# Performance work log

Measured on AMD Instinct MI355X. Metric: run time of the kernel, lower is better.

## Reference

```python
import jax, jax.numpy as jnp
import numpy as np

B, S, E, H, L = 16, 1024, 512, 8, 4
D = E // H  # head_dim = 64


def setup_inputs() -> dict:
    key = jax.random.key(0)
    ks = jax.random.split(key, 16)
    std = 0.02
    inp = {
        "q": jax.random.normal(ks[0], (B, S, E), jnp.float32),
        "k": jax.random.normal(ks[1], (B, S, E), jnp.float32),
        "v": jax.random.normal(ks[2], (B, S, E), jnp.float32),
        # standard Linear params (torch convention: W is (out, in))
        "Wq": jax.random.normal(ks[3], (E, E), jnp.float32) * std,
        "bq": jnp.zeros((E,), jnp.float32),
        "Wk": jax.random.normal(ks[4], (E, E), jnp.float32) * std,
        "bk": jnp.zeros((E,), jnp.float32),
        # WFLinear: shared weight elementwise-multiplied by per-language factor
        "Wv_share": jax.random.normal(ks[5], (E, E), jnp.float32) * std,
        "Wv_spec": 1.0 + jax.random.normal(ks[6], (L, E, E), jnp.float32) * std,
        "bv_share": jnp.zeros((E,), jnp.float32),
        "bv_spec": jax.random.normal(ks[7], (L, E), jnp.float32) * std,
        "Wo_share": jax.random.normal(ks[8], (E, E), jnp.float32) * std,
        "Wo_spec": 1.0 + jax.random.normal(ks[9], (L, E, E), jnp.float32) * std,
        "bo_share": jnp.zeros((E,), jnp.float32),
        "bo_spec": jax.random.normal(ks[10], (L, E), jnp.float32) * std,
        "mask": jax.random.randint(ks[11], (B, S), 0, 2, jnp.int32),
        "languageID": 1,
    }
    return inp


def reference(q, k, v, Wq, bq, Wk, bk, Wv_share, Wv_spec, bv_share, bv_spec,
              Wo_share, Wo_spec, bo_share, bo_spec, mask, languageID):
    scaling = D ** (-0.5)
    # projections (torch Linear: x @ W.T + b)
    Q = (q @ Wq.T + bq).reshape(B, S, H, D).transpose(0, 2, 1, 3) * scaling
    K = (k @ Wk.T + bk).reshape(B, S, H, D).transpose(0, 2, 1, 3)
    Wv = Wv_share * Wv_spec[languageID]
    bv = bv_share + bv_spec[languageID]
    V = (v @ Wv.T + bv).reshape(B, S, H, D).transpose(0, 2, 1, 3)
    # NOTE: faithful to original — Q already scaled by d_k^-0.5, and
    # AttentionWF divides by sqrt(d_k) AGAIN (effective scale 1/d_k).
    alpha = jnp.einsum("bhqd,bhkd->bhqk", Q, K) / np.float32(np.sqrt(D))
    m = (mask == 0)[:, None, None, :]  # (B,1,1,S) over key axis
    alpha = jnp.where(m, jnp.float32(-1e9), alpha)
    alpha = jax.nn.softmax(alpha, axis=-1)
    # dropout p=0.0 -> identity
    ctx = jnp.einsum("bhqk,bhkd->bhqd", alpha, V)  # (B,H,S,D)
    concat = ctx.transpose(0, 2, 1, 3).reshape(B, S, E)
    Wo = Wo_share * Wo_spec[languageID]
    bo = bo_share + bo_spec[languageID]
    return concat @ Wo.T + bo
```

## Files before the change

kernel.cpp:

```cpp
#include <hip/hip_runtime.h>

#define B_ 16
#define S_ 1024
#define E_ 512
#define H_ 8
#define D_ 64
#define L_ 4
#define M_ (B_*S_)

typedef unsigned short u16;
typedef __attribute__((ext_vector_type(8))) short bf16x8;
typedef __attribute__((ext_vector_type(4))) float f32x4;
typedef __attribute__((ext_vector_type(4))) unsigned uint4v;

__device__ __forceinline__ u16 f2bf(float x) {
  unsigned u = __float_as_uint(x);
  unsigned r = (u + 0x7fffu + ((u >> 16) & 1u)) >> 16;
  return (u16)r;
}
__device__ __forceinline__ ushort4 f2bf4(float4 f) {
  ushort4 u;
  u.x = f2bf(f.x); u.y = f2bf(f.y); u.z = f2bf(f.z); u.w = f2bf(f.w);
  return u;
}
__device__ __forceinline__ unsigned cvt_pk_bf16(float lo, float hi) {
  unsigned r;
  asm("v_cvt_pk_bf16_f32 %0, %1, %2" : "=v"(r) : "v"(lo), "v"(hi));
  return r;
}

typedef __attribute__((address_space(1))) const void gconst_void;
typedef __attribute__((address_space(3))) void lds_void;
__device__ __forceinline__ void gl_lds16(const void* g, void* l) {
  __builtin_amdgcn_global_load_lds((gconst_void*)g, (lds_void*)l, 16, 0, 0);
}
__device__ __forceinline__ void fence_vm0_barrier() {
  asm volatile("s_waitcnt vmcnt(0)" ::: "memory");
  __builtin_amdgcn_s_barrier();
}


__global__ __launch_bounds__(256) void prep_w(
    const float* __restrict__ Wq, const float* __restrict__ Wk,
    const float* __restrict__ Wv_sh, const float* __restrict__ Wv_sp,
    const float* __restrict__ Wo_sh, const float* __restrict__ Wo_sp,
    const float* __restrict__ bv_sh, const float* __restrict__ bv_sp,
    const float* __restrict__ bo_sh, const float* __restrict__ bo_sp,
    const int* __restrict__ langp,
    u16* __restrict__ Wq_b, u16* __restrict__ Wk_b,
    u16* __restrict__ Wv_b, u16* __restrict__ Wo_b,
    float* __restrict__ bv_f, float* __restrict__ bo_f) {
  int lang = langp[0];
  int i = blockIdx.x * 256 + threadIdx.x;
  size_t wofs = (size_t)lang * (E_*E_/4) + i;
  ((ushort4*)Wq_b)[i] = f2bf4(((const float4*)Wq)[i]);
  ((ushort4*)Wk_b)[i] = f2bf4(((const float4*)Wk)[i]);
  float4 vs = ((const float4*)Wv_sh)[i], vp = ((const float4*)Wv_sp)[wofs];
  float4 os = ((const float4*)Wo_sh)[i], op = ((const float4*)Wo_sp)[wofs];
  float4 vv = {vs.x*vp.x, vs.y*vp.y, vs.z*vp.z, vs.w*vp.w};
  float4 oo = {os.x*op.x, os.y*op.y, os.z*op.z, os.w*op.w};
  ((ushort4*)Wv_b)[i] = f2bf4(vv);
  ((ushort4*)Wo_b)[i] = f2bf4(oo);
  if (i < E_/4) {
    float4 b1 = ((const float4*)bv_sh)[i], b2 = ((const float4*)(bv_sp + (size_t)lang*E_))[i];
    float4 b3 = ((const float4*)bo_sh)[i], b4 = ((const float4*)(bo_sp + (size_t)lang*E_))[i];
    float4 r1 = {b1.x+b2.x, b1.y+b2.y, b1.z+b2.z, b1.w+b2.w};
    float4 r2 = {b3.x+b4.x, b3.y+b4.y, b3.z+b4.z, b3.w+b4.w};
    ((float4*)bv_f)[i] = r1;
    ((float4*)bo_f)[i] = r2;
  }
}

#define ABBUF 8192
__global__ __launch_bounds__(256, 4) void gemm_qkv(
    const float* __restrict__ q, const float* __restrict__ k, const float* __restrict__ v,
    const u16* __restrict__ Wq_b, const u16* __restrict__ Wk_b, const u16* __restrict__ Wv_b,
    const float* __restrict__ bq, const float* __restrict__ bk, const float* __restrict__ bv,
    u16* __restrict__ Qb, u16* __restrict__ Kb, u16* __restrict__ Vt) {
  __shared__ __align__(16) u16 sA[2*4096];
  __shared__ __align__(16) u16 sB[2*4096];
  const int z = blockIdx.y;
  const float* A    = (z == 0) ? q : (z == 1) ? k : v;
  const u16*   Bw   = (z == 0) ? Wq_b : (z == 1) ? Wk_b : Wv_b;
  const float* bias = (z == 0) ? bq : (z == 1) ? bk : bv;
  const int t = threadIdx.x;
  const int hw = blockIdx.x;
  const int wk = (hw & 7) * 64 + (hw >> 3);
  const int m0 = (wk >> 2) * 128, n0 = (wk & 3) * 128;
  const int lane = t & 63, wid = t >> 6;
  const int m16 = lane & 15, qq = lane >> 4;
  const int wrow = (wid >> 1) * 64, wcol = (wid & 1) * 64;
  const int key = (lane & 7) << 4;
  f32x4 acc[4][4] = {};
  const int arow = t >> 1;
  const float* aR = A + (size_t)(m0 + arow) * E_ + (t & 1) * 16;
  const int awr0 = (arow*64 + (t&1)*32)      ^ ((arow & 7) << 4);
  const int awr1 = (arow*64 + (t&1)*32 + 16) ^ ((arow & 7) << 4);
  const int cb0 = wid*2, cb1 = wid*2 + 1;
  const int rl0 = ((lane>>2)&1) ^ ((lane>>4)&1);
  const int brow = 2*(lane>>3) + rl0;
  const int bcol = (((lane&1)^rl0)<<3) + ((((lane>>1)&1) ^ ((lane>>3)&1))<<4);
  const u16* bp0 = Bw + (size_t)(n0 + cb0*16 + brow) * E_ + bcol;
  const u16* bp1 = Bw + (size_t)(n0 + cb1*16 + brow) * E_ + bcol;
  char* sAb = (char*)sA;
  char* sBb = (char*)sB;
  gl_lds16(bp0, sBb + cb0*1024);
  gl_lds16(bp1, sBb + cb1*1024);
  f32x4 ar0 = *(const f32x4*)aR;
  f32x4 ar1 = *(const f32x4*)(aR + 4);
  f32x4 ar2 = *(const f32x4*)(aR + 8);
  f32x4 ar3 = *(const f32x4*)(aR + 12);
  aR += 32; bp0 += 32; bp1 += 32;
  asm volatile("s_waitcnt vmcnt(0)" ::: "memory");
  {
    uint4v w0 = { cvt_pk_bf16(ar0[0],ar0[1]), cvt_pk_bf16(ar0[2],ar0[3]),
                  cvt_pk_bf16(ar1[0],ar1[1]), cvt_pk_bf16(ar1[2],ar1[3]) };
    uint4v w1 = { cvt_pk_bf16(ar2[0],ar2[1]), cvt_pk_bf16(ar2[2],ar2[3]),
                  cvt_pk_bf16(ar3[0],ar3[1]), cvt_pk_bf16(ar3[2],ar3[3]) };
    *(uint4v*)(sAb + awr0) = w0;
    *(uint4v*)(sAb + awr1) = w1;
  }
  asm volatile("s_waitcnt lgkmcnt(0)" ::: "memory");
  __builtin_amdgcn_s_barrier();
  for (int kt = 0; kt < 16; ++kt) {
    const int cur = (kt & 1) * ABBUF;
    const int nxt = ABBUF - cur;
    if (kt < 15) {
      gl_lds16(bp0, sBb + nxt + cb0*1024);
      gl_lds16(bp1, sBb + nxt + cb1*1024);
      ar0 = *(const f32x4*)aR;
      ar1 = *(const f32x4*)(aR + 4);
      ar2 = *(const f32x4*)(aR + 8);
      ar3 = *(const f32x4*)(aR + 12);
      aR += 32; bp0 += 32; bp1 += 32;
    }
    bf16x8 af[4], bfm[4];
#pragma unroll
    for (int mt = 0; mt < 4; ++mt) {
      int row = wrow + mt*16 + m16;
      af[mt] = *(const bf16x8*)(sAb + cur + ((row*64 + qq*16) ^ key));
    }
#pragma unroll
    for (int nt = 0; nt < 4; ++nt) {
      int row = wcol + nt*16 + m16;
      bfm[nt] = *(const bf16x8*)(sBb + cur + ((row*64 + qq*16) ^ key));
    }
#pragma unroll
    for (int mt = 0; mt < 4; ++mt)
#pragma unroll
      for (int nt = 0; nt < 4; ++nt)
        acc[mt][nt] = __builtin_amdgcn_mfma_f32_16x16x32_bf16(af[mt], bfm[nt], acc[mt][nt], 0, 0, 0);
    if (kt < 15) {
      asm volatile("s_waitcnt vmcnt(0)" ::: "memory");
      uint4v w0 = { cvt_pk_bf16(ar0[0],ar0[1]), cvt_pk_bf16(ar0[2],ar0[3]),
                    cvt_pk_bf16(ar1[0],ar1[1]), cvt_pk_bf16(ar1[2],ar1[3]) };
      uint4v w1 = { cvt_pk_bf16(ar2[0],ar2[1]), cvt_pk_bf16(ar2[2],ar2[3]),
                    cvt_pk_bf16(ar3[0],ar3[1]), cvt_pk_bf16(ar3[2],ar3[3]) };
      *(uint4v*)(sAb + nxt + awr0) = w0;
      *(uint4v*)(sAb + nxt + awr1) = w1;
      asm volatile("s_waitcnt lgkmcnt(0)" ::: "memory");
      __builtin_amdgcn_s_barrier();
    }
  }
  float bvv[4];
#pragma unroll
  for (int nt = 0; nt < 4; ++nt) bvv[nt] = bias[n0 + wcol + nt*16 + m16];
  if (z < 2) {
    u16* out = (z == 0) ? Qb : Kb;
#pragma unroll
    for (int mt = 0; mt < 4; ++mt) {
      int gm = m0 + wrow + mt*16 + qq*4;
#pragma unroll
      for (int nt = 0; nt < 4; ++nt) {
        int gn = n0 + wcol + nt*16 + m16;
#pragma unroll
        for (int r = 0; r < 4; ++r)
          out[(size_t)(gm + r) * E_ + gn] = f2bf(acc[mt][nt][r] + bvv[nt]);
      }
    }
  } else {
#pragma unroll
    for (int mt = 0; mt < 4; ++mt) {
      int tok0 = m0 + wrow + mt*16 + qq*4;
      int bb = tok0 >> 10, s0 = tok0 & 1023;
#pragma unroll
      for (int nt = 0; nt < 4; ++nt) {
        int dim = n0 + wcol + nt*16 + m16;
        uint2 wv = { cvt_pk_bf16(acc[mt][nt][0] + bvv[nt], acc[mt][nt][1] + bvv[nt]),
                     cvt_pk_bf16(acc[mt][nt][2] + bvv[nt], acc[mt][nt][3] + bvv[nt]) };
        *(uint2*)(Vt + ((size_t)(bb*E_ + dim))*S_ + s0) = wv;
      }
    }
  }
}

__global__ __launch_bounds__(256, 4) void gemm_lds(
    const u16* __restrict__ A, const u16* __restrict__ Bw,
    const float* __restrict__ bias, float* __restrict__ out) {
  __shared__ __align__(16) u16 sAD[2*4096];
  __shared__ __align__(16) u16 sBD[2*2048];
  const int t = threadIdx.x;
  const int hw = blockIdx.x;
  const int wk = (hw & 7) * 128 + (hw >> 3);
  const int m0 = (wk >> 3) * 128, n0 = (wk & 7) * 64;
  const int lane = t & 63, wid = t >> 6;
  const int m16 = lane & 15, qq = lane >> 4;
  const int wrow = (wid >> 1) * 64, wcol = (wid & 1) * 32;
  const int key = (lane & 7) << 4;
  f32x4 acc[4][2] = {};
  const int rl0 = ((lane>>2)&1) ^ ((lane>>4)&1);
  const int brow = 2*(lane>>3) + rl0;
  const int bcol = (((lane&1)^rl0)<<3) + ((((lane>>1)&1) ^ ((lane>>3)&1))<<4);
  const int c0 = 2*wid, c1 = 2*wid + 1;
  const u16* a0 = A  + (size_t)(m0 + c0*16 + brow) * E_ + bcol;
  const u16* a1 = A  + (size_t)(m0 + c1*16 + brow) * E_ + bcol;
  const u16* b0 = Bw + (size_t)(n0 + wid*16 + brow) * E_ + bcol;
  char* sAb = (char*)sAD;
  char* sBb = (char*)sBD;
  gl_lds16(a0, sAb + c0*1024);
  gl_lds16(a1, sAb + c1*1024);
  gl_lds16(b0, sBb + wid*1024);
  a0 += 32; a1 += 32; b0 += 32;
  fence_vm0_barrier();
  for (int kt = 0; kt < 16; ++kt) {
    const int curA = (kt & 1) * 8192, nxtA = 8192 - curA;
    const int curB = (kt & 1) * 4096, nxtB = 4096 - curB;
    if (kt < 15) {
      gl_lds16(a0, sAb + nxtA + c0*1024);
      gl_lds16(a1, sAb + nxtA + c1*1024);
      gl_lds16(b0, sBb + nxtB + wid*1024);
      a0 += 32; a1 += 32; b0 += 32;
    }
    bf16x8 af[4], bfm[2];
#pragma unroll
    for (int mt = 0; mt < 4; ++mt) {
      int row = wrow + mt*16 + m16;
      af[mt] = *(const bf16x8*)(sAb + curA + ((row*64 + qq*16) ^ key));
    }
#pragma unroll
    for (int nt = 0; nt < 2; ++nt) {
      int row = wcol + nt*16 + m16;
      bfm[nt] = *(const bf16x8*)(sBb + curB + ((row*64 + qq*16) ^ key));
    }
#pragma unroll
    for (int mt = 0; mt < 4; ++mt)
#pragma unroll
      for (int nt = 0; nt < 2; ++nt)
        acc[mt][nt] = __builtin_amdgcn_mfma_f32_16x16x32_bf16(af[mt], bfm[nt], acc[mt][nt], 0, 0, 0);
    if (kt < 15) fence_vm0_barrier();
  }
  float bv[2];
#pragma unroll
  for (int nt = 0; nt < 2; ++nt) bv[nt] = bias[n0 + wcol + nt*16 + m16];
#pragma unroll
  for (int mt = 0; mt < 4; ++mt) {
    int gm = m0 + wrow + mt*16 + qq*4;
#pragma unroll
    for (int nt = 0; nt < 2; ++nt) {
      int gn = n0 + wcol + nt*16 + m16;
#pragma unroll
      for (int r = 0; r < 4; ++r)
        out[(size_t)(gm + r) * E_ + gn] = acc[mt][nt][r] + bv[nt];
    }
  }
}

#define KST 72
__global__ __launch_bounds__(256) void attn_mfma(
    const u16* __restrict__ Qb, const u16* __restrict__ Kb, const u16* __restrict__ Vt,
    const int* __restrict__ mask, u16* __restrict__ ctxb) {
  __shared__ __align__(16) u16 sK[64*KST];
  __shared__ __align__(16) u16 sV[64*KST];
  __shared__ __align__(16) u16 sP[64*KST];
  __shared__ __align__(16) float sMask[64];
  __shared__ __align__(16) float sL[64];
  const int t = threadIdx.x;
  const int lane = t & 63, w = t >> 6;
  const int m16 = lane & 15, quad = lane >> 4;
  const int hw = blockIdx.x;
  const int wk = (hw & 7) * 256 + (hw >> 3);
  const int bh = wk >> 4, b = bh >> 3, h = bh & 7;
  const int qblk = (wk & 15) * 64;
  const int q0 = qblk + w * 16;
  bf16x8 qf0, qf1;
  {
    const u16* qp = Qb + (size_t)(b*S_ + q0 + m16) * E_ + h*D_ + quad*8;
    qf0 = *(const bf16x8*)qp;
    qf1 = *(const bf16x8*)(qp + 32);
  }
  f32x4 oacc[4] = {};
  float lpart = 0.f;
  const int srow = t >> 2, sc0 = (t & 3) * 16;
  const u16* kp = Kb + (size_t)(b*S_ + srow) * E_ + h*D_ + sc0;
  const u16* vp = Vt + ((size_t)(b*H_ + h) * D_ + srow) * S_ + sc0;
  uint4 rk0 = *(const uint4*)kp, rk1 = *(const uint4*)(kp + 8);
  uint4 rv0 = *(const uint4*)vp, rv1 = *(const uint4*)(vp + 8);
  float rmsk = 0.f;
  if (t < 64) rmsk = (mask[b*S_ + t] == 0) ? -1e9f : 0.f;
  const float CS = 0.015625f * 1.44269504f;
  for (int kt = 0; kt < S_; kt += 64) {
    *(uint4*)&sK[srow*KST + sc0]     = rk0;
    *(uint4*)&sK[srow*KST + sc0 + 8] = rk1;
    *(uint4*)&sV[srow*KST + sc0]     = rv0;
    *(uint4*)&sV[srow*KST + sc0 + 8] = rv1;
    if (t < 64) sMask[t] = rmsk;
    __syncthreads();
    if (kt + 64 < S_) {
      kp += (size_t)64 * E_; vp += 64;
      rk0 = *(const uint4*)kp; rk1 = *(const uint4*)(kp + 8);
      rv0 = *(const uint4*)vp; rv1 = *(const uint4*)(vp + 8);
      if (t < 64) rmsk = (mask[b*S_ + kt + 64 + t] == 0) ? -1e9f : 0.f;
    }
    f32x4 sacc[4] = {};
#pragma unroll
    for (int ct = 0; ct < 4; ++ct) {
      bf16x8 kf0 = *(const bf16x8*)&sK[(ct*16 + m16)*KST + quad*8];
      bf16x8 kf1 = *(const bf16x8*)&sK[(ct*16 + m16)*KST + 32 + quad*8];
      sacc[ct] = __builtin_amdgcn_mfma_f32_16x16x32_bf16(kf0, qf0, sacc[ct], 0, 0, 0);
      sacc[ct] = __builtin_amdgcn_mfma_f32_16x16x32_bf16(kf1, qf1, sacc[ct], 0, 0, 0);
    }
#pragma unroll
    for (int ct = 0; ct < 4; ++ct) {
      f32x4 msk = *(const f32x4*)&sMask[ct*16 + quad*4];
      float p0 = exp2f(fmaf(sacc[ct][0], CS, msk[0]));
      float p1 = exp2f(fmaf(sacc[ct][1], CS, msk[1]));
      float p2 = exp2f(fmaf(sacc[ct][2], CS, msk[2]));
      float p3 = exp2f(fmaf(sacc[ct][3], CS, msk[3]));
      lpart += (p0 + p1) + (p2 + p3);
      uint2 pq = { cvt_pk_bf16(p0, p1), cvt_pk_bf16(p2, p3) };
      *(uint2*)&sP[(w*16 + m16)*KST + ct*16 + quad*4] = pq;
    }
    bf16x8 pf0 = *(const bf16x8*)&sP[(w*16 + m16)*KST + quad*8];
    bf16x8 pf1 = *(const bf16x8*)&sP[(w*16 + m16)*KST + 32 + quad*8];
#pragma unroll
    for (int dt = 0; dt < 4; ++dt) {
      bf16x8 vf0 = *(const bf16x8*)&sV[(dt*16 + m16)*KST + quad*8];
      bf16x8 vf1 = *(const bf16x8*)&sV[(dt*16 + m16)*KST + 32 + quad*8];
      oacc[dt] = __builtin_amdgcn_mfma_f32_16x16x32_bf16(pf0, vf0, oacc[dt], 0, 0, 0);
      oacc[dt] = __builtin_amdgcn_mfma_f32_16x16x32_bf16(pf1, vf1, oacc[dt], 0, 0, 0);
    }
    __syncthreads();
  }
  lpart += __shfl_xor(lpart, 16);
  lpart += __shfl_xor(lpart, 32);
  if (quad == 0) sL[w*16 + m16] = lpart;
  float inv[4];
#pragma unroll
  for (int r = 0; r < 4; ++r) inv[r] = 1.0f / sL[w*16 + quad*4 + r];
#pragma unroll
  for (int dt = 0; dt < 4; ++dt)
#pragma unroll
    for (int r = 0; r < 4; ++r)
      sP[(w*16 + quad*4 + r)*KST + dt*16 + m16] = f2bf(oacc[dt][r] * inv[r]);
  __syncthreads();
  const int orow = t >> 2, oc0 = (t & 3) * 16;
  uint4 o0 = *(uint4*)&sP[orow*KST + oc0];
  uint4 o1 = *(uint4*)&sP[orow*KST + oc0 + 8];
  u16* dst = ctxb + (size_t)(b*S_ + qblk + orow) * E_ + h*D_ + oc0;
  *(uint4*)dst = o0;
  *(uint4*)(dst + 8) = o1;
}

extern "C" void kernel_launch(void* const* d_in, const int* in_sizes, int n_in,
                              void* d_out, int out_size, void* d_ws, size_t ws_size,
                              hipStream_t stream) {
  const float* q     = (const float*)d_in[0];
  const float* k     = (const float*)d_in[1];
  const float* v     = (const float*)d_in[2];
  const float* Wq    = (const float*)d_in[3];
  const float* bq    = (const float*)d_in[4];
  const float* Wk    = (const float*)d_in[5];
  const float* bk    = (const float*)d_in[6];
  const float* Wv_sh = (const float*)d_in[7];
  const float* Wv_sp = (const float*)d_in[8];
  const float* bv_sh = (const float*)d_in[9];
  const float* bv_sp = (const float*)d_in[10];
  const float* Wo_sh = (const float*)d_in[11];
  const float* Wo_sp = (const float*)d_in[12];
  const float* bo_sh = (const float*)d_in[13];
  const float* bo_sp = (const float*)d_in[14];
  const int*   mask  = (const int*)d_in[15];
  const int*   lang  = (const int*)d_in[16];

  char* ws = (char*)d_ws;
  size_t off = 0;
  auto alloc = [&](size_t bytes) -> char* {
    char* p = ws + off;
    off += (bytes + 255) & ~(size_t)255;
    return p;
  };
  u16* Qb   = (u16*)alloc((size_t)M_ * E_ * 2);
  u16* Kb   = (u16*)alloc((size_t)M_ * E_ * 2);
  u16* Vt   = (u16*)alloc((size_t)M_ * E_ * 2);
  u16* ctxb = (u16*)alloc((size_t)M_ * E_ * 2);
  u16* Wq_b = (u16*)alloc((size_t)E_ * E_ * 2);
  u16* Wk_b = (u16*)alloc((size_t)E_ * E_ * 2);
  u16* Wv_b = (u16*)alloc((size_t)E_ * E_ * 2);
  u16* Wo_b = (u16*)alloc((size_t)E_ * E_ * 2);
  float* bv_f = (float*)alloc(E_ * 4);
  float* bo_f = (float*)alloc(E_ * 4);

  prep_w<<<E_*E_/1024, 256, 0, stream>>>(Wq, Wk, Wv_sh, Wv_sp, Wo_sh, Wo_sp,
                                         bv_sh, bv_sp, bo_sh, bo_sp, lang,
                                         Wq_b, Wk_b, Wv_b, Wo_b, bv_f, bo_f);

  dim3 qkvgrid(512, 3);
  gemm_qkv<<<qkvgrid, 256, 0, stream>>>(q, k, v, Wq_b, Wk_b, Wv_b,
                                        bq, bk, bv_f, Qb, Kb, Vt);

  attn_mfma<<<2048, 256, 0, stream>>>(Qb, Kb, Vt, mask, ctxb);

  gemm_lds<<<1024, 256, 0, stream>>>(ctxb, Wo_b, bo_f, (float*)d_out);
}
```

Baseline: 302.0 us.

## Use 32x32x16 MFMA in attention with register P via permlane32 swap

The attention kernel moves from 16x16x32 to 32x32x16 bf16 MFMA, so each wave now handles 32 query rows and a block covers 128 queries, halving the grid. The softmax probabilities are rearranged into the A-operand layout in registers with permlane32_swap instead of a round trip through shared memory, which removes the sP buffer. Each K/V tile loaded into LDS is therefore reused by twice as many queries. The cost is more accumulator registers per wave, which may lower occupancy, and fewer blocks to spread across the GPU.

```diff
diff --git a/kernel.cpp b/kernel.cpp
--- a/kernel.cpp
+++ b/kernel.cpp
@@ -11,7 +11,9 @@
 typedef unsigned short u16;
 typedef __attribute__((ext_vector_type(8))) short bf16x8;
 typedef __attribute__((ext_vector_type(4))) float f32x4;
+typedef __attribute__((ext_vector_type(16))) float f32x16;
 typedef __attribute__((ext_vector_type(4))) unsigned uint4v;
+typedef __attribute__((ext_vector_type(2))) int int2v;
 
 __device__ __forceinline__ u16 f2bf(float x) {
   unsigned u = __float_as_uint(x);
@@ -28,6 +30,9 @@
   asm("v_cvt_pk_bf16_f32 %0, %1, %2" : "=v"(r) : "v"(lo), "v"(hi));
   return r;
 }
+__device__ __forceinline__ int2v plswap(unsigned x, unsigned y) {
+  return __builtin_amdgcn_permlane32_swap((int)x, (int)y, false, false);
+}
 
 typedef __attribute__((address_space(1))) const void gconst_void;
 typedef __attribute__((address_space(3))) void lds_void;
@@ -38,7 +43,6 @@
   asm volatile("s_waitcnt vmcnt(0)" ::: "memory");
   __builtin_amdgcn_s_barrier();
 }
-
 
 __global__ __launch_bounds__(256) void prep_w(
     const float* __restrict__ Wq, const float* __restrict__ Wk,
@@ -269,26 +273,26 @@
 __global__ __launch_bounds__(256) void attn_mfma(
     const u16* __restrict__ Qb, const u16* __restrict__ Kb, const u16* __restrict__ Vt,
     const int* __restrict__ mask, u16* __restrict__ ctxb) {
-  __shared__ __align__(16) u16 sK[64*KST];
-  __shared__ __align__(16) u16 sV[64*KST];
-  __shared__ __align__(16) u16 sP[64*KST];
+  __shared__ __align__(16) u16 sKV[2*64*KST];
   __shared__ __align__(16) float sMask[64];
-  __shared__ __align__(16) float sL[64];
+  __shared__ __align__(16) float sL[128];
+  u16* sK = sKV;
+  u16* sV = sKV + 64*KST;
   const int t = threadIdx.x;
   const int lane = t & 63, w = t >> 6;
-  const int m16 = lane & 15, quad = lane >> 4;
+  const int l31 = lane & 31, lh = lane >> 5;
   const int hw = blockIdx.x;
-  const int wk = (hw & 7) * 256 + (hw >> 3);
-  const int bh = wk >> 4, b = bh >> 3, h = bh & 7;
-  const int qblk = (wk & 15) * 64;
-  const int q0 = qblk + w * 16;
-  bf16x8 qf0, qf1;
+  const int wk = (hw & 7) * 128 + (hw >> 3);
+  const int bh = wk >> 3, b = bh >> 3, h = bh & 7;
+  const int qblk = (wk & 7) * 128;
+  const int q0 = qblk + w * 32;
+  bf16x8 qfr[4];
   {
-    const u16* qp = Qb + (size_t)(b*S_ + q0 + m16) * E_ + h*D_ + quad*8;
-    qf0 = *(const bf16x8*)qp;
-    qf1 = *(const bf16x8*)(qp + 32);
-  }
-  f32x4 oacc[4] = {};
+    const u16* qp = Qb + (size_t)(b*S_ + q0 + l31) * E_ + h*D_ + lh*8;
+#pragma unroll
+    for (int s = 0; s < 4; ++s) qfr[s] = *(const bf16x8*)(qp + s*16);
+  }
+  f32x16 oacc[2] = {};
   float lpart = 0.f;
   const int srow = t >> 2, sc0 = (t & 3) * 16;
   const u16* kp = Kb + (size_t)(b*S_ + srow) * E_ + h*D_ + sc0;
@@ -311,54 +315,71 @@
       rv0 = *(const uint4*)vp; rv1 = *(const uint4*)(vp + 8);
       if (t < 64) rmsk = (mask[b*S_ + kt + 64 + t] == 0) ? -1e9f : 0.f;
     }
-    f32x4 sacc[4] = {};
-#pragma unroll
-    for (int ct = 0; ct < 4; ++ct) {
-      bf16x8 kf0 = *(const bf16x8*)&sK[(ct*16 + m16)*KST + quad*8];
-      bf16x8 kf1 = *(const bf16x8*)&sK[(ct*16 + m16)*KST + 32 + quad*8];
-      sacc[ct] = __builtin_amdgcn_mfma_f32_16x16x32_bf16(kf0, qf0, sacc[ct], 0, 0, 0);
-      sacc[ct] = __builtin_amdgcn_mfma_f32_16x16x32_bf16(kf1, qf1, sacc[ct], 0, 0, 0);
-    }
-#pragma unroll
-    for (int ct = 0; ct < 4; ++ct) {
-      f32x4 msk = *(const f32x4*)&sMask[ct*16 + quad*4];
-      float p0 = exp2f(fmaf(sacc[ct][0], CS, msk[0]));
-      float p1 = exp2f(fmaf(sacc[ct][1], CS, msk[1]));
-      float p2 = exp2f(fmaf(sacc[ct][2], CS, msk[2]));
-      float p3 = exp2f(fmaf(sacc[ct][3], CS, msk[3]));
-      lpart += (p0 + p1) + (p2 + p3);
-      uint2 pq = { cvt_pk_bf16(p0, p1), cvt_pk_bf16(p2, p3) };
-      *(uint2*)&sP[(w*16 + m16)*KST + ct*16 + quad*4] = pq;
-    }
-    bf16x8 pf0 = *(const bf16x8*)&sP[(w*16 + m16)*KST + quad*8];
-    bf16x8 pf1 = *(const bf16x8*)&sP[(w*16 + m16)*KST + 32 + quad*8];
-#pragma unroll
-    for (int dt = 0; dt < 4; ++dt) {
-      bf16x8 vf0 = *(const bf16x8*)&sV[(dt*16 + m16)*KST + quad*8];
-      bf16x8 vf1 = *(const bf16x8*)&sV[(dt*16 + m16)*KST + 32 + quad*8];
-      oacc[dt] = __builtin_amdgcn_mfma_f32_16x16x32_bf16(pf0, vf0, oacc[dt], 0, 0, 0);
-      oacc[dt] = __builtin_amdgcn_mfma_f32_16x16x32_bf16(pf1, vf1, oacc[dt], 0, 0, 0);
+    f32x16 sacc[2] = {};
+#pragma unroll
+    for (int mt = 0; mt < 2; ++mt)
+#pragma unroll
+      for (int s = 0; s < 4; ++s) {
+        bf16x8 kf = *(const bf16x8*)&sK[(mt*32 + l31)*KST + s*16 + lh*8];
+        sacc[mt] = __builtin_amdgcn_mfma_f32_32x32x16_bf16(kf, qfr[s], sacc[mt], 0, 0, 0);
+      }
+    unsigned pw[2][4][2];
+#pragma unroll
+    for (int mt = 0; mt < 2; ++mt)
+#pragma unroll
+      for (int g = 0; g < 4; ++g) {
+        f32x4 msk = *(const f32x4*)&sMask[mt*32 + g*8 + lh*4];
+        float p0 = exp2f(fmaf(sacc[mt][4*g+0], CS, msk[0]));
+        float p1 = exp2f(fmaf(sacc[mt][4*g+1], CS, msk[1]));
+        float p2 = exp2f(fmaf(sacc[mt][4*g+2], CS, msk[2]));
+        float p3 = exp2f(fmaf(sacc[mt][4*g+3], CS, msk[3]));
+        lpart += (p0 + p1) + (p2 + p3);
+        pw[mt][g][0] = cvt_pk_bf16(p0, p1);
+        pw[mt][g][1] = cvt_pk_bf16(p2, p3);
+      }
+#pragma unroll
+    for (int s = 0; s < 4; ++s) {
+      const int mt = s >> 1, c = s & 1;
+      int2v P1 = plswap(pw[mt][2*c][0], pw[mt][2*c+1][0]);
+      int2v P2 = plswap(pw[mt][2*c][1], pw[mt][2*c+1][1]);
+      union { uint4v u; bf16x8 h8; } pa;
+      pa.u = (uint4v){ (unsigned)P1[0], (unsigned)P2[0], (unsigned)P1[1], (unsigned)P2[1] };
+#pragma unroll
+      for (int nt = 0; nt < 2; ++nt) {
+        bf16x8 vf = *(const bf16x8*)&sV[(nt*32 + l31)*KST + s*16 + lh*8];
+        oacc[nt] = __builtin_amdgcn_mfma_f32_32x32x16_bf16(pa.h8, vf, oacc[nt], 0, 0, 0);
+      }
     }
     __syncthreads();
   }
-  lpart += __shfl_xor(lpart, 16);
   lpart += __shfl_xor(lpart, 32);
-  if (quad == 0) sL[w*16 + m16] = lpart;
-  float inv[4];
-#pragma unroll
-  for (int r = 0; r < 4; ++r) inv[r] = 1.0f / sL[w*16 + quad*4 + r];
-#pragma unroll
-  for (int dt = 0; dt < 4; ++dt)
-#pragma unroll
-    for (int r = 0; r < 4; ++r)
-      sP[(w*16 + quad*4 + r)*KST + dt*16 + m16] = f2bf(oacc[dt][r] * inv[r]);
+  if (lane < 32) sL[w*32 + l31] = lpart;
+  f32x4 linv[4];
+#pragma unroll
+  for (int g = 0; g < 4; ++g) {
+    f32x4 lv = *(const f32x4*)&sL[w*32 + 8*g + 4*lh];
+    linv[g] = (f32x4){1.0f/lv[0], 1.0f/lv[1], 1.0f/lv[2], 1.0f/lv[3]};
+  }
+#pragma unroll
+  for (int nt = 0; nt < 2; ++nt)
+#pragma unroll
+    for (int g = 0; g < 4; ++g)
+#pragma unroll
+      for (int r2 = 0; r2 < 4; ++r2) {
+        int qoff = 8*g + 4*lh + r2;
+        sKV[(w*32 + qoff)*KST + nt*32 + l31] = f2bf(oacc[nt][4*g+r2] * linv[g][r2]);
+      }
   __syncthreads();
-  const int orow = t >> 2, oc0 = (t & 3) * 16;
-  uint4 o0 = *(uint4*)&sP[orow*KST + oc0];
-  uint4 o1 = *(uint4*)&sP[orow*KST + oc0 + 8];
-  u16* dst = ctxb + (size_t)(b*S_ + qblk + orow) * E_ + h*D_ + oc0;
+  const int row = t >> 1, c0 = (t & 1) * 32;
+  uint4 o0 = *(uint4*)&sKV[row*KST + c0];
+  uint4 o1 = *(uint4*)&sKV[row*KST + c0 + 8];
+  uint4 o2 = *(uint4*)&sKV[row*KST + c0 + 16];
+  uint4 o3 = *(uint4*)&sKV[row*KST + c0 + 24];
+  u16* dst = ctxb + (size_t)(b*S_ + qblk + row) * E_ + h*D_ + c0;
   *(uint4*)dst = o0;
-  *(uint4*)(dst + 8) = o1;
+  *(uint4*)(dst + 8)  = o1;
+  *(uint4*)(dst + 16) = o2;
+  *(uint4*)(dst + 24) = o3;
 }
 
 extern "C" void kernel_launch(void* const* d_in, const int* in_sizes, int n_in,
@@ -408,7 +429,7 @@
   gemm_qkv<<<qkvgrid, 256, 0, stream>>>(q, k, v, Wq_b, Wk_b, Wv_b,
                                         bq, bk, bv_f, Qb, Kb, Vt);
 
-  attn_mfma<<<2048, 256, 0, stream>>>(Qb, Kb, Vt, mask, ctxb);
+  attn_mfma<<<1024, 256, 0, stream>>>(Qb, Kb, Vt, mask, ctxb);
 
   gemm_lds<<<1024, 256, 0, stream>>>(ctxb, Wo_b, bo_f, (float*)d_out);
 }
```

After: 301.8 us. Within noise of the previous version (-0.1%).
